# Kernel tuning notes

Measured on AMD Instinct MI355X. Metric: run time of the kernel, lower is better.

The kernel has to match this reference:

```python
import jax, jax.numpy as jnp
import numpy as np

B, S, D_IN, M, H, F, L, D_OUT = 4, 1024, 256, 1024, 16, 8, 2, 256
HD = M // H
EPS = 1e-5


def setup_inputs() -> dict:
    key = jax.random.key(0)
    ks = iter(jax.random.split(key, 40))
    w = lambda *s: 0.02 * jax.random.normal(next(ks), s, dtype=jnp.float32)
    inp = {
        "x": jax.random.normal(next(ks), (B, S, D_IN), dtype=jnp.float32),
        # phase embedding params
        "Wemb": w(D_IN, M), "bemb": w(M),
        "Wamp": w(M, F), "bamp": w(F),
        "freqs": jnp.logspace(-1, 2, F, dtype=jnp.float32),
        "phase_off": w(F),
        # per-layer attention params, stacked on leading L axis
        "Wq": w(L, M, M), "bq": w(L, M),
        "Wk": w(L, M, M), "bk": w(L, M),
        "Wv": w(L, M, M), "bv": w(L, M),
        "Wo": w(L, M, M), "bo": w(L, M),
        "pbias": w(L, H, F),
        "ln_g": jnp.ones((L, M), dtype=jnp.float32),
        "ln_b": jnp.zeros((L, M), dtype=jnp.float32),
        # output projection MLP
        "W1": w(M, M // 2), "b1": w(M // 2),
        "W2": w(M // 2, D_OUT), "b2": w(D_OUT),
    }
    return inp


def _forward(x, Wemb, bemb, Wamp, bamp, freqs, phase_off,
             Wq, bq, Wk, bk, Wv, bv, Wo, bo, pbias, ln_g, ln_b,
             W1, b1, W2, b2):
    Bsz, Seq, _ = x.shape
    # --- TemporalPhaseEmbedding ---
    m = x @ Wemb + bemb                                   # [B,S,M]
    tc = jnp.arange(Seq, dtype=x.dtype) / Seq * (2.0 * jnp.pi)  # [S]
    amp = jax.nn.softmax(m @ Wamp + bamp, axis=-1)        # [B,S,F]
    pc = tc[:, None] * freqs[None, :] + phase_off         # [S,F] (batch-identical)
    # |m[...,None] * amp * e^{i*pc}| averaged over F == |m| * mean_F(amp)
    pf = jnp.abs(m) * jnp.mean(amp, axis=-1, keepdims=True)  # [B,S,M]
    # phase-coherence, batch-independent since pc is shared across batch
    coh = jnp.cos(pc[:, None, :] - pc[None, :, :])        # [S,S,F]
    scale = 1.0 / jnp.sqrt(jnp.asarray(HD, dtype=x.dtype))
    for l in range(L):
        res = pf
        Q = (pf @ Wq[l] + bq[l]).reshape(Bsz, Seq, H, HD)
        K = (pf @ Wk[l] + bk[l]).reshape(Bsz, Seq, H, HD)
        V = (pf @ Wv[l] + bv[l]).reshape(Bsz, Seq, H, HD)
        bias = jnp.einsum('stf,hf->hst', coh, pbias[l])   # [H,S,S]
        scores = jnp.einsum('bshd,bthd->bhst', Q, K) * scale + bias[None]
        w_attn = jax.nn.softmax(scores, axis=-1)
        att = jnp.einsum('bhst,bthd->bshd', w_attn, V).reshape(Bsz, Seq, M)
        att = att @ Wo[l] + bo[l]
        y = att + res
        mu = jnp.mean(y, axis=-1, keepdims=True)
        var = jnp.var(y, axis=-1, keepdims=True)
        pf = (y - mu) / jnp.sqrt(var + EPS) * ln_g[l] + ln_b[l]
    hdn = jax.nn.relu(pf @ W1 + b1)
    return hdn @ W2 + b2                                  # [B,S,D_OUT]


def reference(x, Wemb, bemb, Wamp, bamp, freqs, phase_off,
              Wq, bq, Wk, bk, Wv, bv, Wo, bo, pbias, ln_g, ln_b,
              W1, b1, W2, b2):
    return _forward(x, Wemb, bemb, Wamp, bamp, freqs, phase_off,
                    Wq, bq, Wk, bk, Wv, bv, Wo, bo, pbias, ln_g, ln_b,
                    W1, b1, W2, b2)
```

## Files before the change

### kernel.cpp

```cpp
#include <hip/hip_runtime.h>
#include <cmath>

#define B_    4
#define S_    1024
#define DIN_  256
#define M_    1024
#define H_    16
#define F_    8
#define L_    2
#define DOUT_ 256
#define NT_   4096

typedef unsigned short u16;
typedef unsigned int   u32;
typedef __bf16 bf16x8 __attribute__((ext_vector_type(8)));
typedef float  f32x4  __attribute__((ext_vector_type(4)));

#define LOG2E 1.4426950408889634f
#define QSCALE (0.125f * LOG2E)

__device__ __forceinline__ u16 f2b(float f) {
    u32 u = __builtin_bit_cast(u32, f);
    u += 0x7fffu + ((u >> 16) & 1u);
    return (u16)(u >> 16);
}
__device__ __forceinline__ float b2f(u32 h) {
    return __builtin_bit_cast(float, h << 16);
}
__device__ __forceinline__ void gload_lds16(const void* g, void* l) {
    __builtin_amdgcn_global_load_lds(
        (const __attribute__((address_space(1))) u32*)g,
        (__attribute__((address_space(3))) u32*)l, 16, 0, 0);
}

__device__ __forceinline__ void tileT(float (*t)[33], const float* src,
                                      u16* dst, int K, int N, int n0, int k0,
                                      int tid)
{
    const int r = tid >> 3, c4 = (tid & 7) << 2;
    float4 v = *(const float4*)(src + (size_t)(k0 + r) * N + n0 + c4);
    t[r][c4 + 0] = v.x; t[r][c4 + 1] = v.y; t[r][c4 + 2] = v.z; t[r][c4 + 3] = v.w;
    __syncthreads();
    ushort4 o = make_ushort4(f2b(t[c4 + 0][r]), f2b(t[c4 + 1][r]),
                             f2b(t[c4 + 2][r]), f2b(t[c4 + 3][r]));
    *(ushort4*)(dst + (size_t)(n0 + r) * K + k0 + c4) = o;
}

__global__ __launch_bounds__(256) void prep_k(
    const float* __restrict__ x, const float* __restrict__ Wemb,
    const float* __restrict__ Wq, const float* __restrict__ Wk,
    const float* __restrict__ Wv, const float* __restrict__ Wo,
    const float* __restrict__ W1, const float* __restrict__ W2,
    const float* __restrict__ freqs, const float* __restrict__ poff,
    const float* __restrict__ pb, const float* __restrict__ bq,
    const float* __restrict__ bk, const float* __restrict__ bv,
    u16* __restrict__ xb, u16* __restrict__ WembT, u16* __restrict__ WqkvT,
    u16* __restrict__ WoT, u16* __restrict__ W1T, u16* __restrict__ W2T,
    u16* __restrict__ qcs, u16* __restrict__ csb, float* __restrict__ bqkv)
{
    __shared__ float t[32][33];
    const int bid = blockIdx.x, tid = threadIdx.x;

    if (bid < 1024) {
        int i = (bid * 256 + tid) * 4;
        float4 v = *(const float4*)(x + i);
        *(ushort4*)(xb + i) = make_ushort4(f2b(v.x), f2b(v.y), f2b(v.z), f2b(v.w));
    } else if (bid < 7168) {
        int id = bid - 1024;
        int z = id >> 10, rem = id & 1023;
        int n0 = (rem & 31) << 5, k0 = (rem >> 5) << 5;
        int l = z / 3, which = z - l * 3;
        const float* src = (which == 0 ? Wq : which == 1 ? Wk : Wv) + (size_t)l * M_ * M_;
        u16* d = WqkvT + (size_t)l * 3072 * 1024 + (size_t)which * 1024 * 1024;
        tileT(t, src, d, 1024, 1024, n0, k0, tid);
    } else if (bid < 9216) {
        int id = bid - 7168;
        int z = id >> 10, rem = id & 1023;
        int n0 = (rem & 31) << 5, k0 = (rem >> 5) << 5;
        tileT(t, Wo + (size_t)z * M_ * M_, WoT + (size_t)z * M_ * M_,
              1024, 1024, n0, k0, tid);
    } else if (bid < 9472) {
        int id = bid - 9216;
        int n0 = (id & 31) << 5, k0 = (id >> 5) << 5;
        tileT(t, Wemb, WembT, 256, 1024, n0, k0, tid);
    } else if (bid < 9984) {
        int id = bid - 9472;
        int n0 = (id & 15) << 5, k0 = (id >> 4) << 5;
        tileT(t, W1, W1T, 1024, 512, n0, k0, tid);
    } else if (bid < 10112) {
        int id = bid - 9984;
        int n0 = (id & 7) << 5, k0 = (id >> 3) << 5;
        tileT(t, W2, W2T, 512, 256, n0, k0, tid);
    } else if (bid < 12224) {
        const int QN = L_ * H_ * S_ * 16;
        int idx = (bid - 10112) * 256 + tid;
        if (idx < QN) {
            int f2 = idx & 15, f = f2 & 7;
            int s = (idx >> 4) & 1023;
            int lh = idx >> 14;
            float pc = ((float)s * (6.283185307179586f / 1024.f)) * freqs[f] + poff[f];
            float v = (f2 < 8) ? cosf(pc) : sinf(pc);
            qcs[idx] = f2b(pb[lh * 8 + f] * v * LOG2E);
        } else {
            int i2 = idx - QN;
            int f2 = i2 & 15, f = f2 & 7;
            int s = i2 >> 4;
            float pc = ((float)s * (6.283185307179586f / 1024.f)) * freqs[f] + poff[f];
            csb[i2] = f2b((f2 < 8) ? cosf(pc) : sinf(pc));
        }
    } else {
        int idx = (bid - 12224) * 256 + tid;
        int l = idx >= 3072;
        int j = idx - l * 3072;
        float v = (j < 1024) ? bq[l * 1024 + j]
                : (j < 2048) ? bk[l * 1024 + j - 1024]
                             : bv[l * 1024 + j - 2048];
        bqkv[idx] = v;
    }
}

template<int EPI, int OUTBF>
__global__ __launch_bounds__(256, 2) void mgemm_k(
    const u16* __restrict__ A, const u16* __restrict__ Wt,
    const float* __restrict__ bias, void* __restrict__ Cout,
    u16* __restrict__ vt, int N, int K)
{
    __shared__ __attribute__((aligned(16))) u16 As[128 * 64];
    __shared__ __attribute__((aligned(16))) u16 Bs[128 * 64];
    const int tid = threadIdx.x;
    const int lane = tid & 63;
    const int bn = blockIdx.x, bm = blockIdx.y;
    const int wid = tid >> 6, wr = wid >> 1, wc = wid & 1;

    f32x4 acc[4][4];
#pragma unroll
    for (int m = 0; m < 4; ++m)
#pragma unroll
        for (int n = 0; n < 4; ++n) {
            f32x4 z = {0.f, 0.f, 0.f, 0.f};
            acc[m][n] = z;
        }

    const int r = lane & 15, g = lane >> 4;
    const int nk = K >> 6;

    for (int kt = 0; kt < nk; ++kt) {
        const int k0 = kt << 6;
        __syncthreads();
#pragma unroll
        for (int i = 0; i < 4; ++i) {
            int slot = i * 256 + tid;
            int row = slot >> 3;
            int kg = (slot & 7) ^ (row & 7);
            gload_lds16(A + (size_t)(bm * 128 + row) * K + k0 + kg * 8,
                        As + (size_t)(slot & ~63) * 8);
        }
#pragma unroll
        for (int i = 0; i < 4; ++i) {
            int slot = i * 256 + tid;
            int row = slot >> 3;
            int kg = (slot & 7) ^ (row & 7);
            gload_lds16(Wt + (size_t)(bn * 128 + row) * K + k0 + kg * 8,
                        Bs + (size_t)(slot & ~63) * 8);
        }
        __syncthreads();

#pragma unroll
        for (int ks = 0; ks < 2; ++ks) {
            bf16x8 af[4], bfr[4];
#pragma unroll
            for (int m = 0; m < 4; ++m) {
                int row = wr * 64 + m * 16 + r;
                int kg = (ks * 4 + g) ^ (row & 7);
                af[m] = *(const bf16x8*)(As + row * 64 + kg * 8);
            }
#pragma unroll
            for (int n = 0; n < 4; ++n) {
                int row = wc * 64 + n * 16 + r;
                int kg = (ks * 4 + g) ^ (row & 7);
                bfr[n] = *(const bf16x8*)(Bs + row * 64 + kg * 8);
            }
#pragma unroll
            for (int m = 0; m < 4; ++m)
#pragma unroll
                for (int n = 0; n < 4; ++n)
                    acc[m][n] = __builtin_amdgcn_mfma_f32_16x16x32_bf16(
                        af[m], bfr[n], acc[m][n], 0, 0, 0);
        }
    }

#pragma unroll
    for (int n = 0; n < 4; ++n) {
        const int gcol = bn * 128 + wc * 64 + n * 16 + r;
        const float bb = bias[gcol];
#pragma unroll
        for (int m = 0; m < 4; ++m) {
            const int grow0 = bm * 128 + wr * 64 + m * 16 + g * 4;
            if (EPI == 5 && gcol >= 2048) {
                int d = gcol - 2048;
                int bh = (grow0 >> 10) * 16 + (d >> 6);
                u16 pk[4];
#pragma unroll
                for (int q = 0; q < 4; ++q) pk[q] = f2b(acc[m][n][q] + bb);
                uint2 pv;
                pv.x = (u32)pk[0] | ((u32)pk[1] << 16);
                pv.y = (u32)pk[2] | ((u32)pk[3] << 16);
                *(uint2*)(vt + ((size_t)bh * 64 + (d & 63)) * 1024 + (grow0 & 1023)) = pv;
            } else {
#pragma unroll
                for (int q = 0; q < 4; ++q) {
                    float c = acc[m][n][q] + bb;
                    if (EPI == 1) c = fabsf(c) * 0.125f;
                    if (EPI == 2) c = fmaxf(c, 0.f);
                    if (EPI == 5) c = (gcol < 1024) ? c * QSCALE : c;
                    if (OUTBF)
                        ((u16*)Cout)[(size_t)(grow0 + q) * N + gcol] = f2b(c);
                    else
                        ((float*)Cout)[(size_t)(grow0 + q) * N + gcol] = c;
                }
            }
        }
    }
}

__global__ __launch_bounds__(256) void fattn_k(
    const u16* __restrict__ QKV, const u16* __restrict__ Vtg,
    const u16* __restrict__ csb, const u16* __restrict__ qcs,
    u16* __restrict__ Og)
{
    __shared__ __attribute__((aligned(16))) u16 Ks2[2][64 * 64];
    __shared__ __attribute__((aligned(16))) u16 Vt2[2][64 * 64];
    __shared__ __attribute__((aligned(16))) u16 Ext[2][64 * 16];
    __shared__ __attribute__((aligned(16))) u16 Pl[4][32 * 68];
    const int tid = threadIdx.x, lane = tid & 63, w = tid >> 6;
    const int c = lane & 15, g = lane >> 4;
    const int h = blockIdx.y, b = blockIdx.z, bh = b * 16 + h;
    const int s0 = blockIdx.x * 128;

    const uint4 zz = {0u, 0u, 0u, 0u};
    const bf16x8 zfrag = __builtin_bit_cast(bf16x8, zz);

    bf16x8 aq[2][3];
#pragma unroll
    for (int m = 0; m < 2; ++m) {
        int sl = s0 + w * 32 + m * 16 + c;
        size_t tok = (size_t)b * 1024 + sl;
        aq[m][0] = *(const bf16x8*)(QKV + tok * 3072 + h * 64 + g * 8);
        aq[m][1] = *(const bf16x8*)(QKV + tok * 3072 + h * 64 + 32 + g * 8);
        aq[m][2] = (g < 2) ? *(const bf16x8*)(qcs + ((size_t)h * 1024 + sl) * 16 + g * 8)
                           : zfrag;
    }

    f32x4 oacc[2][4];
#pragma unroll
    for (int m = 0; m < 2; ++m)
#pragma unroll
        for (int n = 0; n < 4; ++n) {
            f32x4 z = {0.f, 0.f, 0.f, 0.f};
            oacc[m][n] = z;
        }
    float lsum[2] = {0.f, 0.f};

    auto STAGE = [&](int buf, int t0) {
#pragma unroll
        for (int i = 0; i < 2; ++i) {
            int slot = i * 256 + tid;
            int row = slot >> 3, gi = slot & 7;
            int kg = (gi ^ (row & 7)) * 8;
            gload_lds16(QKV + (size_t)(b * 1024 + t0 + row) * 3072 + 1024 + h * 64 + kg,
                        &Ks2[buf][(size_t)(slot & ~63) * 8]);
            gload_lds16(Vtg + (size_t)(bh * 64 + row) * 1024 + t0 + kg,
                        &Vt2[buf][(size_t)(slot & ~63) * 8]);
        }
        if (tid < 128) {
            int r2 = tid >> 1, g2 = tid & 1;
            gload_lds16(csb + (size_t)(t0 + r2) * 16 + g2 * 8,
                        &Ext[buf][(size_t)(tid & ~63) * 8]);
        }
    };

    STAGE(0, 0);
    __builtin_amdgcn_sched_barrier(0);

    for (int it = 0; it < 16; ++it) {
        const int cur = it & 1;
        if (it < 15) {
            STAGE(cur ^ 1, (it + 1) << 6);
            if (w < 2) asm volatile("s_waitcnt vmcnt(5)" ::: "memory");
            else       asm volatile("s_waitcnt vmcnt(4)" ::: "memory");
        } else {
            asm volatile("s_waitcnt vmcnt(0)" ::: "memory");
        }
        __builtin_amdgcn_sched_barrier(0);
        __builtin_amdgcn_s_barrier();
        __builtin_amdgcn_sched_barrier(0);

        f32x4 sacc[2][4];
#pragma unroll
        for (int m = 0; m < 2; ++m)
#pragma unroll
            for (int n = 0; n < 4; ++n) {
                f32x4 z = {0.f, 0.f, 0.f, 0.f};
                sacc[m][n] = z;
            }
        __builtin_amdgcn_s_setprio(1);
#pragma unroll
        for (int ks = 0; ks < 3; ++ks) {
            bf16x8 bk[4];
#pragma unroll
            for (int n = 0; n < 4; ++n) {
                int tr = n * 16 + c;
                if (ks < 2) {
                    int kg = (ks * 4 + g) ^ (tr & 7);
                    bk[n] = *(const bf16x8*)(&Ks2[cur][tr * 64 + kg * 8]);
                } else {
                    bk[n] = (g < 2) ? *(const bf16x8*)(&Ext[cur][tr * 16 + g * 8]) : zfrag;
                }
            }
#pragma unroll
            for (int n = 0; n < 4; ++n)
#pragma unroll
                for (int m = 0; m < 2; ++m)
                    sacc[m][n] = __builtin_amdgcn_mfma_f32_16x16x32_bf16(
                        bk[n], aq[m][ks], sacc[m][n], 0, 0, 0);
        }
        __builtin_amdgcn_s_setprio(0);

#pragma unroll
        for (int m = 0; m < 2; ++m)
#pragma unroll
            for (int n = 0; n < 4; ++n) {
                u16 pk[4];
#pragma unroll
                for (int q = 0; q < 4; ++q) {
                    float p = __builtin_amdgcn_exp2f(sacc[m][n][q]);
                    lsum[m] += p;
                    pk[q] = f2b(p);
                }
                uint2 pv;
                pv.x = (u32)pk[0] | ((u32)pk[1] << 16);
                pv.y = (u32)pk[2] | ((u32)pk[3] << 16);
                *(uint2*)(&Pl[w][(m * 16 + c) * 68 + n * 16 + g * 4]) = pv;
            }

        __builtin_amdgcn_s_setprio(1);
#pragma unroll
        for (int ks2 = 0; ks2 < 2; ++ks2) {
            bf16x8 pa[2];
#pragma unroll
            for (int m = 0; m < 2; ++m)
                pa[m] = *(const bf16x8*)(&Pl[w][(m * 16 + c) * 68 + ks2 * 32 + g * 8]);
#pragma unroll
            for (int n = 0; n < 4; ++n) {
                int dr = n * 16 + c;
                int kg = (ks2 * 4 + g) ^ (dr & 7);
                bf16x8 vf = *(const bf16x8*)(&Vt2[cur][dr * 64 + kg * 8]);
#pragma unroll
                for (int m = 0; m < 2; ++m)
                    oacc[m][n] = __builtin_amdgcn_mfma_f32_16x16x32_bf16(
                        pa[m], vf, oacc[m][n], 0, 0, 0);
            }
        }
        __builtin_amdgcn_s_setprio(0);

        __builtin_amdgcn_sched_barrier(0);
        __builtin_amdgcn_s_barrier();
        __builtin_amdgcn_sched_barrier(0);
    }

#pragma unroll
    for (int m = 0; m < 2; ++m) {
        float lt = lsum[m] + __shfl_xor(lsum[m], 16);
        lt += __shfl_xor(lt, 32);
        float inv[4];
#pragma unroll
        for (int q = 0; q < 4; ++q)
            inv[q] = 1.f / __shfl(lt, g * 4 + q);
#pragma unroll
        for (int n = 0; n < 4; ++n)
#pragma unroll
            for (int q = 0; q < 4; ++q) {
                size_t tok = (size_t)b * 1024 + s0 + w * 32 + m * 16 + g * 4 + q;
                Og[tok * 1024 + h * 64 + n * 16 + c] = f2b(oacc[m][n][q] * inv[q]);
            }
    }
}

__global__ __launch_bounds__(256) void ln_k(
    const u16* __restrict__ Y, u16* __restrict__ Pf,
    const float* __restrict__ g, const float* __restrict__ bt)
{
    const int rw = blockIdx.x;
    const int tid = threadIdx.x;
    const u16* yp = Y + (size_t)rw * M_ + tid * 4;
    u16* pp = Pf + (size_t)rw * M_ + tid * 4;
    ushort4 yv = *(const ushort4*)yp;
    ushort4 rv = *(const ushort4*)pp;
    float a[4];
    a[0] = b2f(yv.x) + b2f(rv.x); a[1] = b2f(yv.y) + b2f(rv.y);
    a[2] = b2f(yv.z) + b2f(rv.z); a[3] = b2f(yv.w) + b2f(rv.w);
    float s = a[0] + a[1] + a[2] + a[3];
    float q = a[0] * a[0] + a[1] * a[1] + a[2] * a[2] + a[3] * a[3];
#pragma unroll
    for (int o = 1; o < 64; o <<= 1) {
        s += __shfl_xor(s, o);
        q += __shfl_xor(q, o);
    }
    __shared__ float ss[4], qq[4];
    if ((tid & 63) == 0) { ss[tid >> 6] = s; qq[tid >> 6] = q; }
    __syncthreads();
    s = ss[0] + ss[1] + ss[2] + ss[3];
    q = qq[0] + qq[1] + qq[2] + qq[3];
    float mu = s * (1.0f / 1024.0f);
    float var = q * (1.0f / 1024.0f) - mu * mu;
    float inv = rsqrtf(var + 1e-5f);
    float4 gv = *(const float4*)(g + (tid << 2));
    float4 bv = *(const float4*)(bt + (tid << 2));
    *(ushort4*)pp = make_ushort4(
        f2b((a[0] - mu) * inv * gv.x + bv.x),
        f2b((a[1] - mu) * inv * gv.y + bv.y),
        f2b((a[2] - mu) * inv * gv.z + bv.z),
        f2b((a[3] - mu) * inv * gv.w + bv.w));
}

extern "C" void kernel_launch(void* const* d_in, const int* in_sizes, int n_in,
                              void* d_out, int out_size, void* d_ws, size_t ws_size,
                              hipStream_t stream)
{
    const float* x     = (const float*)d_in[0];
    const float* Wemb  = (const float*)d_in[1];
    const float* bemb  = (const float*)d_in[2];
    const float* freqs = (const float*)d_in[5];
    const float* poff  = (const float*)d_in[6];
    const float* Wq    = (const float*)d_in[7];
    const float* bq    = (const float*)d_in[8];
    const float* Wk    = (const float*)d_in[9];
    const float* bk    = (const float*)d_in[10];
    const float* Wv    = (const float*)d_in[11];
    const float* bv    = (const float*)d_in[12];
    const float* Wo    = (const float*)d_in[13];
    const float* bo    = (const float*)d_in[14];
    const float* pbias = (const float*)d_in[15];
    const float* lng   = (const float*)d_in[16];
    const float* lnb   = (const float*)d_in[17];
    const float* W1    = (const float*)d_in[18];
    const float* b1    = (const float*)d_in[19];
    const float* W2    = (const float*)d_in[20];
    const float* b2    = (const float*)d_in[21];
    float* out = (float*)d_out;

    char* ws = (char*)d_ws;
    const size_t MB = 1 << 20;
    u16* pf    = (u16*)(ws);
    u16* QKV   = (u16*)(ws + 8 * MB);
    u16* Ab    = (u16*)(ws + 32 * MB);
    u16* Vtg   = (u16*)(ws + 40 * MB);
    u16* WqkvT = (u16*)(ws + 48 * MB);
    u16* WoT   = (u16*)(ws + 60 * MB);
    u16* WembT = (u16*)(ws + 64 * MB);
    u16* W1T   = (u16*)(ws + 64 * MB + 512 * 1024);
    u16* W2T   = (u16*)(ws + 65 * MB + 512 * 1024);
    u16* xb    = (u16*)(ws + 66 * MB);
    u16* qcs   = (u16*)(ws + 68 * MB);
    u16* csb   = (u16*)(ws + 69 * MB);
    float* bqkv = (float*)(ws + 69 * MB + 64 * 1024);

    dim3 blk(256);
    prep_k<<<12248, blk, 0, stream>>>(x, Wemb, Wq, Wk, Wv, Wo, W1, W2,
                                      freqs, poff, pbias, bq, bk, bv,
                                      xb, WembT, WqkvT, WoT, W1T, W2T,
                                      qcs, csb, bqkv);

    mgemm_k<1, 1><<<dim3(8, 32), blk, 0, stream>>>(xb, WembT, bemb, pf, nullptr, 1024, 256);

    for (int l = 0; l < L_; ++l) {
        mgemm_k<5, 1><<<dim3(24, 32), blk, 0, stream>>>(
            pf, WqkvT + (size_t)l * 3072 * 1024, bqkv + l * 3072, QKV, Vtg, 3072, 1024);
        fattn_k<<<dim3(8, 16, 4), blk, 0, stream>>>(
            QKV, Vtg, csb, qcs + (size_t)l * H_ * S_ * 16, Ab);
        mgemm_k<0, 1><<<dim3(8, 32), blk, 0, stream>>>(
            Ab, WoT + (size_t)l * M_ * M_, bo + l * M_, QKV , nullptr, 1024, 1024);
        ln_k<<<dim3(NT_), blk, 0, stream>>>(QKV, pf, lng + l * M_, lnb + l * M_);
    }

    mgemm_k<2, 1><<<dim3(4, 32), blk, 0, stream>>>(pf, W1T, b1, Ab, nullptr, 512, 1024);
    mgemm_k<0, 0><<<dim3(2, 32), blk, 0, stream>>>(Ab, W2T, b2, out, nullptr, 256, 512);
}
```

Measured before the change: 252.4 us.

## Triple-buffer attention K/V staging and remap blocks for XCD locality

Moves the flash-attention kernel from double to triple buffering of K, V^T and the phase-extension tiles, prefetching two tiles ahead with adjusted vmcnt waits to hide global-load latency better. It also flattens the grid to 1D and remaps block ids so the eight query tiles of one (batch, head) pair fall on the same XCD, aiming for better L2 reuse of K/V. The softmax probability packing now uses native bf16 conversion with a tree sum instead of manual rounding. The costs are more LDS per block, which may reduce occupancy, and the block mapping assumes a round-robin dispatch of blocks across XCDs.

```diff
diff --git a/kernel.cpp b/kernel.cpp
--- a/kernel.cpp
+++ b/kernel.cpp
@@ -14,6 +14,7 @@
 typedef unsigned short u16;
 typedef unsigned int   u32;
 typedef __bf16 bf16x8 __attribute__((ext_vector_type(8)));
+typedef __bf16 bf16x4v __attribute__((ext_vector_type(4)));
 typedef float  f32x4  __attribute__((ext_vector_type(4)));
 
 #define LOG2E 1.4426950408889634f
@@ -228,14 +229,18 @@
     const u16* __restrict__ csb, const u16* __restrict__ qcs,
     u16* __restrict__ Og)
 {
-    __shared__ __attribute__((aligned(16))) u16 Ks2[2][64 * 64];
-    __shared__ __attribute__((aligned(16))) u16 Vt2[2][64 * 64];
-    __shared__ __attribute__((aligned(16))) u16 Ext[2][64 * 16];
+    __shared__ __attribute__((aligned(16))) u16 Ks3[3][64 * 64];
+    __shared__ __attribute__((aligned(16))) u16 Vt3[3][64 * 64];
+    __shared__ __attribute__((aligned(16))) u16 Ext[3][64 * 16];
     __shared__ __attribute__((aligned(16))) u16 Pl[4][32 * 68];
     const int tid = threadIdx.x, lane = tid & 63, w = tid >> 6;
     const int c = lane & 15, g = lane >> 4;
-    const int h = blockIdx.y, b = blockIdx.z, bh = b * 16 + h;
-    const int s0 = blockIdx.x * 128;
+    const int Lid = blockIdx.x;
+    const int slot = Lid >> 3;
+    const int grp = (Lid & 7) * 8 + (slot >> 3);
+    const int qi = slot & 7;
+    const int b = grp >> 4, h = grp & 15, bh = grp;
+    const int s0 = qi * 128;
 
     const uint4 zz = {0u, 0u, 0u, 0u};
     const bf16x8 zfrag = __builtin_bit_cast(bf16x8, zz);
@@ -250,6 +255,7 @@
         aq[m][2] = (g < 2) ? *(const bf16x8*)(qcs + ((size_t)h * 1024 + sl) * 16 + g * 8)
                            : zfrag;
     }
+    __builtin_amdgcn_sched_barrier(0);
 
     f32x4 oacc[2][4];
 #pragma unroll
@@ -264,13 +270,13 @@
     auto STAGE = [&](int buf, int t0) {
 #pragma unroll
         for (int i = 0; i < 2; ++i) {
-            int slot = i * 256 + tid;
-            int row = slot >> 3, gi = slot & 7;
+            int sl2 = i * 256 + tid;
+            int row = sl2 >> 3, gi = sl2 & 7;
             int kg = (gi ^ (row & 7)) * 8;
             gload_lds16(QKV + (size_t)(b * 1024 + t0 + row) * 3072 + 1024 + h * 64 + kg,
-                        &Ks2[buf][(size_t)(slot & ~63) * 8]);
+                        &Ks3[buf][(size_t)(sl2 & ~63) * 8]);
             gload_lds16(Vtg + (size_t)(bh * 64 + row) * 1024 + t0 + kg,
-                        &Vt2[buf][(size_t)(slot & ~63) * 8]);
+                        &Vt3[buf][(size_t)(sl2 & ~63) * 8]);
         }
         if (tid < 128) {
             int r2 = tid >> 1, g2 = tid & 1;
@@ -280,12 +286,17 @@
     };
 
     STAGE(0, 0);
+    STAGE(1, 64);
     __builtin_amdgcn_sched_barrier(0);
 
+    int cur = 0;
     for (int it = 0; it < 16; ++it) {
-        const int cur = it & 1;
-        if (it < 15) {
-            STAGE(cur ^ 1, (it + 1) << 6);
+        if (it < 14) {
+            int nb = cur + 2; if (nb >= 3) nb -= 3;
+            STAGE(nb, (it + 2) << 6);
+            if (w < 2) asm volatile("s_waitcnt vmcnt(10)" ::: "memory");
+            else       asm volatile("s_waitcnt vmcnt(8)" ::: "memory");
+        } else if (it == 14) {
             if (w < 2) asm volatile("s_waitcnt vmcnt(5)" ::: "memory");
             else       asm volatile("s_waitcnt vmcnt(4)" ::: "memory");
         } else {
@@ -295,6 +306,10 @@
         __builtin_amdgcn_s_barrier();
         __builtin_amdgcn_sched_barrier(0);
 
+        const u16* ksb = &Ks3[cur][0];
+        const u16* vtb = &Vt3[cur][0];
+        const u16* exb = &Ext[cur][0];
+
         f32x4 sacc[2][4];
 #pragma unroll
         for (int m = 0; m < 2; ++m)
@@ -312,9 +327,9 @@
                 int tr = n * 16 + c;
                 if (ks < 2) {
                     int kg = (ks * 4 + g) ^ (tr & 7);
-                    bk[n] = *(const bf16x8*)(&Ks2[cur][tr * 64 + kg * 8]);
+                    bk[n] = *(const bf16x8*)(ksb + tr * 64 + kg * 8);
                 } else {
-                    bk[n] = (g < 2) ? *(const bf16x8*)(&Ext[cur][tr * 16 + g * 8]) : zfrag;
+                    bk[n] = (g < 2) ? *(const bf16x8*)(exb + tr * 16 + g * 8) : zfrag;
                 }
             }
 #pragma unroll
@@ -330,17 +345,15 @@
         for (int m = 0; m < 2; ++m)
 #pragma unroll
             for (int n = 0; n < 4; ++n) {
-                u16 pk[4];
-#pragma unroll
-                for (int q = 0; q < 4; ++q) {
-                    float p = __builtin_amdgcn_exp2f(sacc[m][n][q]);
-                    lsum[m] += p;
-                    pk[q] = f2b(p);
-                }
-                uint2 pv;
-                pv.x = (u32)pk[0] | ((u32)pk[1] << 16);
-                pv.y = (u32)pk[2] | ((u32)pk[3] << 16);
-                *(uint2*)(&Pl[w][(m * 16 + c) * 68 + n * 16 + g * 4]) = pv;
+                float p0 = __builtin_amdgcn_exp2f(sacc[m][n][0]);
+                float p1 = __builtin_amdgcn_exp2f(sacc[m][n][1]);
+                float p2 = __builtin_amdgcn_exp2f(sacc[m][n][2]);
+                float p3 = __builtin_amdgcn_exp2f(sacc[m][n][3]);
+                lsum[m] += (p0 + p1) + (p2 + p3);
+                bf16x4v pk;
+                pk[0] = (__bf16)p0; pk[1] = (__bf16)p1;
+                pk[2] = (__bf16)p2; pk[3] = (__bf16)p3;
+                *(bf16x4v*)(&Pl[w][(m * 16 + c) * 68 + n * 16 + g * 4]) = pk;
             }
 
         __builtin_amdgcn_s_setprio(1);
@@ -354,7 +367,7 @@
             for (int n = 0; n < 4; ++n) {
                 int dr = n * 16 + c;
                 int kg = (ks2 * 4 + g) ^ (dr & 7);
-                bf16x8 vf = *(const bf16x8*)(&Vt2[cur][dr * 64 + kg * 8]);
+                bf16x8 vf = *(const bf16x8*)(vtb + dr * 64 + kg * 8);
 #pragma unroll
                 for (int m = 0; m < 2; ++m)
                     oacc[m][n] = __builtin_amdgcn_mfma_f32_16x16x32_bf16(
@@ -366,6 +379,7 @@
         __builtin_amdgcn_sched_barrier(0);
         __builtin_amdgcn_s_barrier();
         __builtin_amdgcn_sched_barrier(0);
+        cur = (cur == 2) ? 0 : cur + 1;
     }
 
 #pragma unroll
@@ -476,7 +490,7 @@
     for (int l = 0; l < L_; ++l) {
         mgemm_k<5, 1><<<dim3(24, 32), blk, 0, stream>>>(
             pf, WqkvT + (size_t)l * 3072 * 1024, bqkv + l * 3072, QKV, Vtg, 3072, 1024);
-        fattn_k<<<dim3(8, 16, 4), blk, 0, stream>>>(
+        fattn_k<<<dim3(512), blk, 0, stream>>>(
             QKV, Vtg, csb, qcs + (size_t)l * H_ * S_ * 16, Ab);
         mgemm_k<0, 1><<<dim3(8, 32), blk, 0, stream>>>(
             Ab, WoT + (size_t)l * M_ * M_, bo + l * M_, QKV , nullptr, 1024, 1024);
```

New measurement: 246.5 us. 1.02x faster.
